# Kernel tuning notes

Measured on AMD Instinct MI355X. Metric: run time of the kernel, lower is better.

Reference implementation:

```python
import jax, jax.numpy as jnp
import numpy as np

B, HIST, PRED, N, E, FEAT = 16, 8, 12, 2000, 64000, 13
IN_DIM = FEAT + 1          # 14 (pm25 concat features)
HID, GNN_OUT, EH, EOUT = 64, 13, 32, 30


def setup_inputs() -> dict:
    key = jax.random.key(0)
    ks = jax.random.split(key, 14)
    pm25_hist = jax.random.normal(ks[0], (B, HIST, N, 1), jnp.float32)
    feature = jax.random.normal(ks[1], (B, HIST + PRED, N, FEAT), jnp.float32)
    edge_index = jax.random.randint(ks[2], (2, E), 0, N)
    dist = jax.random.uniform(ks[3], (E,), minval=10.0, maxval=500.0)
    direc = jax.random.uniform(ks[4], (E,), minval=0.0, maxval=360.0)
    edge_attr = jnp.stack([dist, direc], axis=-1).astype(jnp.float32)  # [E,2]
    wind_mean = jnp.array([3.0, 180.0], jnp.float32)
    wind_std = jnp.array([2.0, 100.0], jnp.float32)

    def w(k, shape):
        return (jax.random.normal(k, shape, jnp.float32) * 0.1)

    return {
        "pm25_hist": pm25_hist, "feature": feature,
        "edge_attr": edge_attr, "wind_mean": wind_mean, "wind_std": wind_std,
        "We1": w(ks[5], (2 * IN_DIM + 3, EH)), "be1": jnp.zeros((EH,), jnp.float32),
        "We2": w(ks[6], (EH, EOUT)), "be2": jnp.zeros((EOUT,), jnp.float32),
        "Wn": w(ks[7], (EOUT, GNN_OUT)), "bn": jnp.zeros((GNN_OUT,), jnp.float32),
        "W1": w(ks[8], (IN_DIM + GNN_OUT, HID)), "b1": jnp.zeros((HID,), jnp.float32),
        "W2": w(ks[9], (HID, HID)), "b2": jnp.zeros((HID,), jnp.float32),
        "W3": w(ks[10], (HID, HID)), "b3": jnp.zeros((HID,), jnp.float32),
        "Wo": w(ks[11], (HID, 1)), "bo": jnp.zeros((1,), jnp.float32),
        "edge_index": edge_index,
    }


def reference(pm25_hist, feature, edge_attr, wind_mean, wind_std,
              We1, be1, We2, be2, Wn, bn, W1, b1, W2, b2, W3, b3, Wo, bo,
              edge_index):
    src, tgt = edge_index[0], edge_index[1]
    # edge_attr normalization computed once at init in the torch module (unbiased std)
    attr_norm = (edge_attr - edge_attr.mean(0)) / edge_attr.std(0, ddof=1)  # [E,2]
    bsz, n_nodes = pm25_hist.shape[0], pm25_hist.shape[2]
    hist_len = pm25_hist.shape[1]
    n_edges = src.shape[0]

    def graph_gnn(x):  # x: [B,N,IN_DIM]
        ns = x[:, src]   # [B,E,D] gather
        nt = x[:, tgt]   # [B,E,D]
        wind = ns[..., -2:] * wind_std + wind_mean          # de-normalize wind feats
        speed, wdir = wind[..., 0], wind[..., 1]
        theta = jnp.abs(edge_attr[:, 1] - wdir)             # |city_direc - wind_direc|
        ew = jax.nn.relu(3.0 * speed * jnp.cos(theta) / edge_attr[:, 0])  # [B,E]
        an = jnp.broadcast_to(attr_norm, (bsz, n_edges, 2))
        e = jnp.concatenate([ns, nt, an, ew[..., None]], axis=-1)  # [B,E,2D+3]
        e = jax.nn.sigmoid(e @ We1 + be1)
        e = jax.nn.sigmoid(e @ We2 + be2)                    # [B,E,EOUT]
        z = jnp.zeros((bsz, n_nodes, e.shape[-1]), e.dtype)
        agg = z.at[:, tgt].add(e) - z.at[:, src].add(e)      # scatter_add - scatter_add
        return jax.nn.sigmoid(agg @ Wn + bn)                 # [B,N,GNN_OUT]

    feats = jnp.swapaxes(feature[:, hist_len:], 0, 1)        # [PRED,B,N,FEAT]

    def step(xn, ft):
        x = jnp.concatenate([xn, ft], axis=-1)               # [B,N,IN_DIM]
        g = graph_gnn(x)
        h = jnp.concatenate([g, x], axis=-1)                 # [B,N,IN_DIM+GNN_OUT]
        h = jax.nn.sigmoid(h @ W1 + b1)
        h = jax.nn.sigmoid(h @ W2 + b2)
        h = jax.nn.sigmoid(h @ W3 + b3)
        xn_new = h @ Wo + bo                                 # [B,N,1]
        return xn_new, xn_new

    _, preds = jax.lax.scan(step, pm25_hist[:, -1], feats)   # [PRED,B,N,1]
    return jnp.swapaxes(preds, 0, 1)                         # [B,PRED,N,1]
```

## Files before the change

### kernel.cpp

```cpp
#include <hip/hip_runtime.h>
#include <math.h>

#define BB 16
#define HIST 8
#define PRED 12
#define NN 2000
#define NE 64000
#define FEAT 13
#define IN_DIM 14
#define HID 64
#define GNN_OUT 13
#define EH 32
#define EOUT 30
#define EOUT_PAD 32
#define TSTEPS 20
#define EIN 31
#define SB 128

typedef unsigned int uint;
typedef unsigned short ushort;

__device__ __forceinline__ float sigmoidf_(float x) {
    return __builtin_amdgcn_rcpf(1.0f + __expf(-x));
}
// ... 89 lines not shown
    int* off = blockIdx.x ? offS : offT;
    int* cur = blockIdx.x ? curS : curT;
    __shared__ int part[256];
    int tid = threadIdx.x;
    int base = tid * 8;
    int v[8]; int s = 0;
#pragma unroll
    for (int k = 0; k < 8; ++k) {
        int idx = base + k;
        int d = (idx < NN) ? deg[idx] : 0;
        v[k] = d; s += d;
    }
    part[tid] = s;
    __syncthreads();
    for (int offn = 1; offn < 256; offn <<= 1) {
        int x = part[tid];
        int y = (tid >= offn) ? part[tid - offn] : 0;
        __syncthreads();
        part[tid] = x + y;
        __syncthreads();
    }
    int run = (tid > 0) ? part[tid - 1] : 0;
#pragma unroll
    for (int k = 0; k < 8; ++k) {
        int idx = base + k;
        if (idx < NN) { off[idx] = run; cur[idx] = run; }
        run += v[k];
    }
    if (tid == 255) off[NN] = run;
}

__global__ void fill_kernel(const int* __restrict__ edge_index,
                            int* __restrict__ curT, int* __restrict__ curS,
                            int* __restrict__ posT, int* __restrict__ listS_eid) {
    int e = blockIdx.x * 256 + threadIdx.x;
    if (e >= NE) return;
    int tg = edge_index[NE + e], s = edge_index[e];
    int p = atomicAdd(&curT[tg], 1);
    posT[e] = p;
    int q = atomicAdd(&curS[s], 1);
    listS_eid[q] = e;
}

__global__ void map_kernel(const int* __restrict__ listS_eid,
                           const int* __restrict__ posT,
                           int* __restrict__ listS_pos) {
    int k = blockIdx.x * 256 + threadIdx.x;
    if (k >= NE) return;
    listS_pos[k] = posT[listS_eid[k]];
}

__global__ void sort_kernel(const int* __restrict__ edge_index,
                            const float* __restrict__ edge_attr,
                            const int* __restrict__ posT,
                            int* __restrict__ srcT, int* __restrict__ tgT,
                            float* __restrict__ attrT) {
    int e = blockIdx.x * 256 + threadIdx.x;
    if (e >= NE) return;
    int p = posT[e];
    srcT[p] = edge_index[e];
    tgT[p] = edge_index[NE + e];
    attrT[2 * p]     = edge_attr[2 * e];
    attrT[2 * p + 1] = edge_attr[2 * e + 1];
}

__global__ void ce_kernel(const float* __restrict__ attrT,
                          const float* __restrict__ stats,
                          const float* __restrict__ We1,
                          const float* __restrict__ be1,
                          uint* __restrict__ Ce) {
    int p = blockIdx.x * 256 + threadIdx.x;
    if (p >= NE) return;
    float an0 = (attrT[2 * p]     - stats[0]) * stats[1];
    float an1 = (attrT[2 * p + 1] - stats[2]) * stats[3];
    float c[EH];
#pragma unroll
    for (int j = 0; j < EH; ++j)
        c[j] = fmaf(an0, We1[28 * EH + j], fmaf(an1, We1[29 * EH + j], be1[j]));
    uint* dst = Ce + (size_t)p * 16;
#pragma unroll
    for (int q = 0; q < 16; ++q) dst[q] = pack2(c[2 * q], c[2 * q + 1]);
}

__global__ __launch_bounds__(256) void proj_kernel(
    const float* __restrict__ xn, const float* __restrict__ feature,
    const float* __restrict__ We1,
    const float* __restrict__ wind_mean, const float* __restrict__ wind_std,
    uint* __restrict__ Ps, uint* __restrict__ Pt,
    float* __restrict__ spd3, float* __restrict__ wdirA, int t) {
    int i = blockIdx.x * 256 + threadIdx.x;
    if (i >= BB * NN) return;
    int b = i / NN, n = i % NN;
    int ht = HIST + t;
    float x[IN_DIM];
    x[0] = xn[i];
    const float* fr = feature + ((size_t)(b * TSTEPS + ht) * NN + n) * FEAT;
#pragma unroll
    for (int f = 0; f < FEAT; ++f) x[1 + f] = fr[f];

    float ps[EH], pt[EH];
#pragma unroll
    for (int j = 0; j < EH; ++j) { ps[j] = 0.f; pt[j] = 0.f; }
#pragma unroll
    for (int f = 0; f < IN_DIM; ++f) {
        float xv = x[f];
#pragma unroll
        for (int j = 0; j < EH; ++j) {
            ps[j] = fmaf(xv, We1[f * EH + j], ps[j]);
            pt[j] = fmaf(xv, We1[(IN_DIM + f) * EH + j], pt[j]);
        }
    }
    uint* pso = Ps + (size_t)i * 16;
    uint* pto = Pt + (size_t)i * 16;
#pragma unroll
    for (int q = 0; q < 16; ++q) {
        pso[q] = pack2(ps[2 * q], ps[2 * q + 1]);
        pto[q] = pack2(pt[2 * q], pt[2 * q + 1]);
    }
    spd3[i]  = 3.0f * fmaf(x[12], wind_std[0], wind_mean[0]);
    wdirA[i] = fmaf(x[13], wind_std[1], wind_mean[1]);
}

__global__ __launch_bounds__(256) void edge_kernel_v3(
    const uint* __restrict__ Ps, const uint* __restrict__ Pt,
    const uint* __restrict__ Ce,
    const float* __restrict__ We1,
    const float* __restrict__ We2, const float* __restrict__ be2,
    const int* __restrict__ srcT, const int* __restrict__ tgT,
    const float* __restrict__ attrT,
    const float* __restrict__ spd3, const float* __restrict__ wdirA,
    ushort* __restrict__ e_out) {
    int p = blockIdx.x * 256 + threadIdx.x;
    if (p >= NE) return;
    int b = blockIdx.y;
    int s  = srcT[p];
    int tg = tgT[p];
    float dist  = attrT[2 * p];
    float direc = attrT[2 * p + 1];
    float sp3 = spd3[b * NN + s];
    float wd  = wdirA[b * NN + s];
    float theta = fabsf(direc - wd);
    float ew = fmaxf(sp3 * cosf(theta) * __builtin_amdgcn_rcpf(dist), 0.0f);

    const uint4* ps4 = (const uint4*)(Ps + ((size_t)b * NN + s)  * 16);
    const uint4* pt4 = (const uint4*)(Pt + ((size_t)b * NN + tg) * 16);
    const uint4* ce4 = (const uint4*)(Ce + (size_t)p * 16);

    float h[EH];
#pragma unroll
    for (int q = 0; q < 4; ++q) {
        uint4 a = ps4[q], c = pt4[q], d = ce4[q];
        uint av[4] = {a.x, a.y, a.z, a.w};
        uint cv[4] = {c.x, c.y, c.z, c.w};
        uint dv[4] = {d.x, d.y, d.z, d.w};
#pragma unroll
        for (int m = 0; m < 4; ++m) {
            int j = q * 8 + m * 2;
            h[j]     = bflo(av[m]) + bflo(cv[m]) + bflo(dv[m]);
            h[j + 1] = bfhi(av[m]) + bfhi(cv[m]) + bfhi(dv[m]);
        }
    }
#pragma unroll
    for (int j = 0; j < EH; ++j)
        h[j] = sigmoidf_(fmaf(ew, We1[30 * EH + j], h[j]));

    float o[EOUT];
#pragma unroll
    for (int j = 0; j < EOUT; ++j) o[j] = be2[j];
#pragma unroll
    for (int i = 0; i < EH; ++i) {
        float x = h[i];
#pragma unroll
        for (int j = 0; j < EOUT; ++j) o[j] = fmaf(x, We2[i * EOUT + j], o[j]);
    }

    uint w[16];
#pragma unroll
    for (int j = 0; j < 15; ++j)
        w[j] = pack2(sigmoidf_(o[2 * j]), sigmoidf_(o[2 * j + 1]));
    w[15] = 0u;
    uint4* dst = (uint4*)(e_out + ((size_t)b * NE + (size_t)p) * EOUT_PAD);
    dst[0] = make_uint4(w[0],  w[1],  w[2],  w[3]);
    dst[1] = make_uint4(w[4],  w[5],  w[6],  w[7]);
    dst[2] = make_uint4(w[8],  w[9],  w[10], w[11]);
    dst[3] = make_uint4(w[12], w[13], w[14], w[15]);
}

__global__ __launch_bounds__(256) void node_kernel_v4(
    const ushort* __restrict__ e_out,
    const int* __restrict__ offT, const int* __restrict__ offS,
    const int* __restrict__ listS_pos,
    float* __restrict__ xn,
    const float* __restrict__ feature,
    const float* __restrict__ Wn, const float* __restrict__ bn,
    const float* __restrict__ W1, const float* __restrict__ b1,
    const float* __restrict__ W2, const float* __restrict__ b2,
    const float* __restrict__ W3, const float* __restrict__ b3,
    const float* __restrict__ Wo, const float* __restrict__ bo,
    const float* __restrict__ We1,
    const float* __restrict__ wind_mean, const float* __restrict__ wind_std,
    uint* __restrict__ Ps, uint* __restrict__ Pt,
    float* __restrict__ spd3, float* __restrict__ wdirA,
    float* __restrict__ out, int t) {
    int wid  = threadIdx.x >> 6;
    int lane = threadIdx.x & 63;
    int node = blockIdx.x * 4 + wid;
    int b = node / NN, n = node % NN;
    int r = lane >> 2;
    int c = lane & 3;
    int ht = HIST + t;

    const uint4* base4 = (const uint4*)(e_out + (size_t)b * NE * EOUT_PAD);

    float acc[8];
#pragma unroll
    for (int i = 0; i < 8; ++i) acc[i] = 0.0f;

    int k0 = offT[n], k1 = offT[n + 1];
    for (int k = k0 + r; k < k1; k += 16) {
        uint4 v = base4[(size_t)k * 4 + c];
        uint vv[4] = {v.x, v.y, v.z, v.w};
#pragma unroll
        for (int m = 0; m < 4; ++m) {
            acc[2 * m]     += bflo(vv[m]);
            acc[2 * m + 1] += bfhi(vv[m]);
        }
    }
    int q0 = offS[n], q1 = offS[n + 1];
    for (int k = q0 + r; k < q1; k += 16) {
        int row = listS_pos[k];
        uint4 v = base4[(size_t)row * 4 + c];
        uint vv[4] = {v.x, v.y, v.z, v.w};
#pragma unroll
        for (int m = 0; m < 4; ++m) {
            acc[2 * m]     -= bflo(vv[m]);
            acc[2 * m + 1] -= bfhi(vv[m]);
        }
    }
#pragma unroll
    for (int m = 4; m <= 32; m <<= 1) {
#pragma unroll
        for (int i = 0; i < 8; ++i) acc[i] += __shfl_xor(acc[i], m);
    }

    __shared__ float smAgg[4][EOUT_PAD];
    __shared__ float smHin[4][28];
    __shared__ float smH[4][HID];

    if (c == 0 && r < 4) {
#pragma unroll
        for (int i = 0; i < 8; ++i) smAgg[wid][r * 8 + i] = acc[i];
    }
    __syncthreads();

    const float* fr = feature + ((size_t)(b * TSTEPS + ht) * NN + n) * FEAT;
    if (lane < GNN_OUT) {
        float g = bn[lane];
#pragma unroll
        for (int k = 0; k < EOUT; ++k)
            g = fmaf(smAgg[wid][k], Wn[k * GNN_OUT + lane], g);
        smHin[wid][lane] = sigmoidf_(g);
    } else if (lane < GNN_OUT + IN_DIM) {
        smHin[wid][lane] = (lane == GNN_OUT) ? xn[node] : fr[lane - GNN_OUT - 1];
    }
    __syncthreads();

    float v = b1[lane];
#pragma unroll
    for (int k = 0; k < GNN_OUT + IN_DIM; ++k)
        v = fmaf(smHin[wid][k], W1[k * HID + lane], v);
    float hval = sigmoidf_(v);
    smH[wid][lane] = hval;
    __syncthreads();

    v = b2[lane];
#pragma unroll
    for (int k = 0; k < HID; ++k)
        v = fmaf(smH[wid][k], W2[k * HID + lane], v);
    hval = sigmoidf_(v);
    __syncthreads();
    smH[wid][lane] = hval;
    __syncthreads();

    v = b3[lane];
#pragma unroll
    for (int k = 0; k < HID; ++k)
        v = fmaf(smH[wid][k], W3[k * HID + lane], v);
    hval = sigmoidf_(v);

    float partial = hval * Wo[lane];
#pragma unroll
    for (int m = 32; m >= 1; m >>= 1)
        partial += __shfl_xor(partial, m);
    float rr = partial + bo[0];
    if (lane == 0) {
        out[((size_t)(b * PRED + t)) * NN + n] = rr;
        xn[node] = rr;
    }

    if (t < PRED - 1) {
        const float* fr2 = feature + ((size_t)(b * TSTEPS + ht + 1) * NN + n) * FEAT;
        float xv[IN_DIM];
        xv[0] = rr;
#pragma unroll
        for (int f = 0; f < FEAT; ++f) xv[1 + f] = fr2[f];
        int j = lane & 31;
        int rowbase = (lane < 32) ? 0 : IN_DIM;
        float p = 0.0f;
#pragma unroll
        for (int f = 0; f < IN_DIM; ++f)
            p = fmaf(xv[f], We1[(rowbase + f) * EH + j], p);
        float pp = __shfl_xor(p, 1);
        if (!(j & 1)) {
            uint packed = pack2(p, pp);
            uint* dst = (lane < 32 ? Ps : Pt) + (size_t)node * 16;
            dst[j >> 1] = packed;
        }
        if (lane == 0) {
            spd3[node]  = 3.0f * fmaf(xv[12], wind_std[0], wind_mean[0]);
            wdirA[node] = fmaf(xv[13], wind_std[1], wind_mean[1]);
        }
    }
}

__device__ __forceinline__ void compute_edge(
    int b, int e, int t,
    const float* __restrict__ xn, const float* __restrict__ feature,
    const float* __restrict__ edge_attr, const int* __restrict__ edge_index,
    const float* __restrict__ stats,
    const float* __restrict__ wind_mean, const float* __restrict__ wind_std,
    const float* __restrict__ We1, const float* __restrict__ be1,
    const float* __restrict__ We2, const float* __restrict__ be2,
    float* __restrict__ o) {
    int s  = edge_index[e];
    int tg = edge_index[NE + e];
    int ht = HIST + t;
    const float* fs  = feature + ((size_t)(b * TSTEPS + ht) * NN + s)  * FEAT;
    const float* ftg = feature + ((size_t)(b * TSTEPS + ht) * NN + tg) * FEAT;
    float ev[EIN];
    ev[0] = xn[b * NN + s];
#pragma unroll
    for (int f = 0; f < FEAT; ++f) ev[1 + f] = fs[f];
    ev[14] = xn[b * NN + tg];
#pragma unroll
    for (int f = 0; f < FEAT; ++f) ev[15 + f] = ftg[f];
    float dist  = edge_attr[2 * e];
    float direc = edge_attr[2 * e + 1];
    ev[28] = (dist  - stats[0]) * stats[1];
    ev[29] = (direc - stats[2]) * stats[3];
    float speed = ev[12] * wind_std[0] + wind_mean[0];
    float wdir  = ev[13] * wind_std[1] + wind_mean[1];
    float theta = fabsf(direc - wdir);
    float ew    = 3.0f * speed * cosf(theta) / dist;
    ev[30] = fmaxf(ew, 0.0f);
    float h[EH];
// ... 142 lines not shown
    const float* be1 = (const float*)d_in[6];
    const float* We2 = (const float*)d_in[7];
    const float* be2 = (const float*)d_in[8];
    const float* Wn  = (const float*)d_in[9];
    const float* bn  = (const float*)d_in[10];
    const float* W1  = (const float*)d_in[11];
    const float* b1  = (const float*)d_in[12];
    const float* W2  = (const float*)d_in[13];
    const float* b2  = (const float*)d_in[14];
    const float* W3  = (const float*)d_in[15];
    const float* b3  = (const float*)d_in[16];
    const float* Wo  = (const float*)d_in[17];
    const float* bo  = (const float*)d_in[18];
    const int* edge_index = (const int*)d_in[19];
    float* out = (float*)d_out;

    char* ws = (char*)d_ws;
    size_t off = 0;
    auto alloc = [&](size_t bytes) {
        void* p = ws + off;
        off = (off + bytes + 255) & ~(size_t)255;
        return p;
    };
    float*  xn    = (float*)alloc((size_t)BB * NN * sizeof(float));
    float*  stats = (float*)alloc(4 * sizeof(float));
    double* part  = (double*)alloc(4 * SB * sizeof(double));
    int* degT      = (int*)alloc(NN * sizeof(int));
    int* degS      = (int*)alloc(NN * sizeof(int));
    int* offT      = (int*)alloc((NN + 1) * sizeof(int));
    int* offS      = (int*)alloc((NN + 1) * sizeof(int));
    int* curT      = (int*)alloc(NN * sizeof(int));
    int* curS      = (int*)alloc(NN * sizeof(int));
    int* posT      = (int*)alloc(NE * sizeof(int));
    int* listS_eid = (int*)alloc(NE * sizeof(int));
    int* listS_pos = (int*)alloc(NE * sizeof(int));
    size_t v2_mark = off;
    int*   srcT  = (int*)alloc(NE * sizeof(int));
    int*   tgT   = (int*)alloc(NE * sizeof(int));
    float* attrT = (float*)alloc(2 * NE * sizeof(float));
    uint*  Ce    = (uint*)alloc((size_t)NE * 16 * sizeof(uint));
    uint*  Ps    = (uint*)alloc((size_t)BB * NN * 16 * sizeof(uint));
    uint*  Pt    = (uint*)alloc((size_t)BB * NN * 16 * sizeof(uint));
    float* spd3  = (float*)alloc((size_t)BB * NN * sizeof(float));
    float* wdirA = (float*)alloc((size_t)BB * NN * sizeof(float));
    size_t eout_bytes = (size_t)BB * NE * EOUT_PAD * sizeof(ushort);
    bool v3 = (ws_size >= off + eout_bytes);
    ushort* e_out = v3 ? (ushort*)(ws + off) : (ushort*)(ws + v2_mark);

    stats_partial<<<SB, 256, 0, stream>>>(edge_attr, part);
    stats_final<<<1, 128, 0, stream>>>(part, stats);
    init_xn<<<(BB * NN + 255) / 256, 256, 0, stream>>>(pm25, xn);
    hipMemsetAsync(degT, 0, NN * sizeof(int), stream);
    hipMemsetAsync(degS, 0, NN * sizeof(int), stream);
    count_kernel<<<(NE + 255) / 256, 256, 0, stream>>>(edge_index, degT, degS);
    scan2_kernel<<<2, 256, 0, stream>>>(degT, degS, offT, offS, curT, curS);
    fill_kernel<<<(NE + 255) / 256, 256, 0, stream>>>(edge_index, curT, curS, posT, listS_eid);
    map_kernel<<<(NE + 255) / 256, 256, 0, stream>>>(listS_eid, posT, listS_pos);

    if (v3) {
        sort_kernel<<<(NE + 255) / 256, 256, 0, stream>>>(edge_index, edge_attr, posT,
                                                          srcT, tgT, attrT);
        ce_kernel<<<(NE + 255) / 256, 256, 0, stream>>>(attrT, stats, We1, be1, Ce);
        proj_kernel<<<(BB * NN + 255) / 256, 256, 0, stream>>>(
            xn, feature, We1, wind_mean, wind_std, Ps, Pt, spd3, wdirA, 0);
        for (int t = 0; t < PRED; ++t) {
            dim3 eg((NE + 255) / 256, BB);
            edge_kernel_v3<<<eg, 256, 0, stream>>>(Ps, Pt, Ce, We1, We2, be2,
                                                   srcT, tgT, attrT, spd3, wdirA, e_out);
            node_kernel_v4<<<BB * NN / 4, 256, 0, stream>>>(
                e_out, offT, offS, listS_pos, xn, feature,
                Wn, bn, W1, b1, W2, b2, W3, b3, Wo, bo,
                We1, wind_mean, wind_std, Ps, Pt, spd3, wdirA, out, t);
        }
    } else {
        for (int t = 0; t < PRED; ++t) {
            dim3 eg((NE + 255) / 256, BB);
            edge_kernel_v2<<<eg, 256, 0, stream>>>(xn, feature, edge_attr, edge_index,
                                                   stats, wind_mean, wind_std,
                                                   We1, be1, We2, be2, posT, e_out, t);
            node_kernel_v2<<<(BB * NN + 255) / 256, 256, 0, stream>>>(
                e_out, offT, offS, listS_pos, xn, feature,
                Wn, bn, W1, b1, W2, b2, W3, b3, Wo, bo, out, t);
        }
    }
}
```

Measured before the change: 1.859 ms.

## Write edge outputs in both target- and source-sorted order for contiguous scatter reads

The edge kernel now writes each edge's packed output twice: once in target-sorted order and once at its source-sorted position, using a new per-edge position map built during CSR construction. The node kernel then reads the subtracted source-side contributions contiguously rather than through the listS_pos indirection. This removes the random gather in the node aggregation. In exchange it doubles edge-output write traffic and workspace use, and it only takes effect when the workspace is large enough.

```diff
diff --git a/kernel.cpp b/kernel.cpp
--- a/kernel.cpp
+++ b/kernel.cpp
@@ -145,13 +145,15 @@
 
 __global__ void fill_kernel(const int* __restrict__ edge_index,
                             int* __restrict__ curT, int* __restrict__ curS,
-                            int* __restrict__ posT, int* __restrict__ listS_eid) {
+                            int* __restrict__ posT, int* __restrict__ posS,
+                            int* __restrict__ listS_eid) {
     int e = blockIdx.x * 256 + threadIdx.x;
     if (e >= NE) return;
     int tg = edge_index[NE + e], s = edge_index[e];
     int p = atomicAdd(&curT[tg], 1);
     posT[e] = p;
     int q = atomicAdd(&curS[s], 1);
+    posS[e] = q;
     listS_eid[q] = e;
 }
 
@@ -165,9 +167,9 @@
 
 __global__ void sort_kernel(const int* __restrict__ edge_index,
                             const float* __restrict__ edge_attr,
-                            const int* __restrict__ posT,
+                            const int* __restrict__ posT, const int* __restrict__ posS,
                             int* __restrict__ srcT, int* __restrict__ tgT,
-                            float* __restrict__ attrT) {
+                            float* __restrict__ attrT, int* __restrict__ pSrc) {
     int e = blockIdx.x * 256 + threadIdx.x;
     if (e >= NE) return;
     int p = posT[e];
@@ -175,6 +177,7 @@
     tgT[p] = edge_index[NE + e];
     attrT[2 * p]     = edge_attr[2 * e];
     attrT[2 * p + 1] = edge_attr[2 * e + 1];
+    pSrc[p] = posS[e];
 }
 
 __global__ void ce_kernel(const float* __restrict__ attrT,
@@ -232,6 +235,89 @@
     }
     spd3[i]  = 3.0f * fmaf(x[12], wind_std[0], wind_mean[0]);
     wdirA[i] = fmaf(x[13], wind_std[1], wind_mean[1]);
+}
+
+__device__ __forceinline__ void edge_mlp(
+    int p, int b, int s, int tg,
+    const uint* __restrict__ Ps, const uint* __restrict__ Pt,
+    const uint* __restrict__ Ce,
+    const float* __restrict__ We1,
+    const float* __restrict__ We2, const float* __restrict__ be2,
+    const float* __restrict__ attrT,
+    const float* __restrict__ spd3, const float* __restrict__ wdirA,
+    uint* __restrict__ w ) {
+    float dist  = attrT[2 * p];
+    float direc = attrT[2 * p + 1];
+    float sp3 = spd3[b * NN + s];
+    float wd  = wdirA[b * NN + s];
+    float theta = fabsf(direc - wd);
+    float ew = fmaxf(sp3 * cosf(theta) * __builtin_amdgcn_rcpf(dist), 0.0f);
+
+    const uint4* ps4 = (const uint4*)(Ps + ((size_t)b * NN + s)  * 16);
+    const uint4* pt4 = (const uint4*)(Pt + ((size_t)b * NN + tg) * 16);
+    const uint4* ce4 = (const uint4*)(Ce + (size_t)p * 16);
+
+    float h[EH];
+#pragma unroll
+    for (int q = 0; q < 4; ++q) {
+        uint4 a = ps4[q], c = pt4[q], d = ce4[q];
+        uint av[4] = {a.x, a.y, a.z, a.w};
+        uint cv[4] = {c.x, c.y, c.z, c.w};
+        uint dv[4] = {d.x, d.y, d.z, d.w};
+#pragma unroll
+        for (int m = 0; m < 4; ++m) {
+            int j = q * 8 + m * 2;
+            h[j]     = bflo(av[m]) + bflo(cv[m]) + bflo(dv[m]);
+            h[j + 1] = bfhi(av[m]) + bfhi(cv[m]) + bfhi(dv[m]);
+        }
+    }
+#pragma unroll
+    for (int j = 0; j < EH; ++j)
+        h[j] = sigmoidf_(fmaf(ew, We1[30 * EH + j], h[j]));
+
+    float o[EOUT];
+#pragma unroll
+    for (int j = 0; j < EOUT; ++j) o[j] = be2[j];
+#pragma unroll
+    for (int i = 0; i < EH; ++i) {
+        float x = h[i];
+#pragma unroll
+        for (int j = 0; j < EOUT; ++j) o[j] = fmaf(x, We2[i * EOUT + j], o[j]);
+    }
+#pragma unroll
+    for (int j = 0; j < 15; ++j)
+        w[j] = pack2(sigmoidf_(o[2 * j]), sigmoidf_(o[2 * j + 1]));
+    w[15] = 0u;
+}
+
+__global__ __launch_bounds__(256) void edge_kernel_v5(
+    const uint* __restrict__ Ps, const uint* __restrict__ Pt,
+    const uint* __restrict__ Ce,
+    const float* __restrict__ We1,
+    const float* __restrict__ We2, const float* __restrict__ be2,
+    const int* __restrict__ srcT, const int* __restrict__ tgT,
+    const int* __restrict__ pSrc,
+    const float* __restrict__ attrT,
+    const float* __restrict__ spd3, const float* __restrict__ wdirA,
+    ushort* __restrict__ e_outT, ushort* __restrict__ e_outS) {
+    int p = blockIdx.x * 256 + threadIdx.x;
+    if (p >= NE) return;
+    int b = blockIdx.y;
+    int s  = srcT[p];
+    int tg = tgT[p];
+    uint w[16];
+    edge_mlp(p, b, s, tg, Ps, Pt, Ce, We1, We2, be2, attrT, spd3, wdirA, w);
+    uint4* dstT = (uint4*)(e_outT + ((size_t)b * NE + (size_t)p) * EOUT_PAD);
+    dstT[0] = make_uint4(w[0],  w[1],  w[2],  w[3]);
+    dstT[1] = make_uint4(w[4],  w[5],  w[6],  w[7]);
+    dstT[2] = make_uint4(w[8],  w[9],  w[10], w[11]);
+    dstT[3] = make_uint4(w[12], w[13], w[14], w[15]);
+    int q = pSrc[p];
+    uint4* dstS = (uint4*)(e_outS + ((size_t)b * NE + (size_t)q) * EOUT_PAD);
+    dstS[0] = make_uint4(w[0],  w[1],  w[2],  w[3]);
+    dstS[1] = make_uint4(w[4],  w[5],  w[6],  w[7]);
+    dstS[2] = make_uint4(w[8],  w[9],  w[10], w[11]);
+    dstS[3] = make_uint4(w[12], w[13], w[14], w[15]);
 }
 
 __global__ __launch_bounds__(256) void edge_kernel_v3(
@@ -248,55 +334,169 @@
     int b = blockIdx.y;
     int s  = srcT[p];
     int tg = tgT[p];
-    float dist  = attrT[2 * p];
-    float direc = attrT[2 * p + 1];
-    float sp3 = spd3[b * NN + s];
-    float wd  = wdirA[b * NN + s];
-    float theta = fabsf(direc - wd);
-    float ew = fmaxf(sp3 * cosf(theta) * __builtin_amdgcn_rcpf(dist), 0.0f);
-
-    const uint4* ps4 = (const uint4*)(Ps + ((size_t)b * NN + s)  * 16);
-    const uint4* pt4 = (const uint4*)(Pt + ((size_t)b * NN + tg) * 16);
-    const uint4* ce4 = (const uint4*)(Ce + (size_t)p * 16);
-
-    float h[EH];
-#pragma unroll
-    for (int q = 0; q < 4; ++q) {
-        uint4 a = ps4[q], c = pt4[q], d = ce4[q];
-        uint av[4] = {a.x, a.y, a.z, a.w};
-        uint cv[4] = {c.x, c.y, c.z, c.w};
-        uint dv[4] = {d.x, d.y, d.z, d.w};
-#pragma unroll
-        for (int m = 0; m < 4; ++m) {
-            int j = q * 8 + m * 2;
-            h[j]     = bflo(av[m]) + bflo(cv[m]) + bflo(dv[m]);
-            h[j + 1] = bfhi(av[m]) + bfhi(cv[m]) + bfhi(dv[m]);
-        }
-    }
-#pragma unroll
-    for (int j = 0; j < EH; ++j)
-        h[j] = sigmoidf_(fmaf(ew, We1[30 * EH + j], h[j]));
-
-    float o[EOUT];
-#pragma unroll
-    for (int j = 0; j < EOUT; ++j) o[j] = be2[j];
-#pragma unroll
-    for (int i = 0; i < EH; ++i) {
-        float x = h[i];
-#pragma unroll
-        for (int j = 0; j < EOUT; ++j) o[j] = fmaf(x, We2[i * EOUT + j], o[j]);
-    }
-
     uint w[16];
-#pragma unroll
-    for (int j = 0; j < 15; ++j)
-        w[j] = pack2(sigmoidf_(o[2 * j]), sigmoidf_(o[2 * j + 1]));
-    w[15] = 0u;
+    edge_mlp(p, b, s, tg, Ps, Pt, Ce, We1, We2, be2, attrT, spd3, wdirA, w);
     uint4* dst = (uint4*)(e_out + ((size_t)b * NE + (size_t)p) * EOUT_PAD);
     dst[0] = make_uint4(w[0],  w[1],  w[2],  w[3]);
     dst[1] = make_uint4(w[4],  w[5],  w[6],  w[7]);
     dst[2] = make_uint4(w[8],  w[9],  w[10], w[11]);
     dst[3] = make_uint4(w[12], w[13], w[14], w[15]);
+}
+
+__device__ __forceinline__ void node_tail(
+    int node, int b, int n, int t, int wid, int lane,
+    float accv[8], int r, int c,
+    float* __restrict__ xn, const float* __restrict__ feature,
+    const float* __restrict__ Wn, const float* __restrict__ bn,
+    const float* __restrict__ W1, const float* __restrict__ b1,
+    const float* __restrict__ W2, const float* __restrict__ b2,
+    const float* __restrict__ W3, const float* __restrict__ b3,
+    const float* __restrict__ Wo, const float* __restrict__ bo,
+    const float* __restrict__ We1,
+    const float* __restrict__ wind_mean, const float* __restrict__ wind_std,
+    uint* __restrict__ Ps, uint* __restrict__ Pt,
+    float* __restrict__ spd3, float* __restrict__ wdirA,
+    float* __restrict__ out,
+    float (*smAgg)[EOUT_PAD], float (*smHin)[28], float (*smH)[HID]) {
+    int ht = HIST + t;
+#pragma unroll
+    for (int m = 4; m <= 32; m <<= 1) {
+#pragma unroll
+        for (int i = 0; i < 8; ++i) accv[i] += __shfl_xor(accv[i], m);
+    }
+    if (c == 0 && r < 4) {
+#pragma unroll
+        for (int i = 0; i < 8; ++i) smAgg[wid][r * 8 + i] = accv[i];
+    }
+    __syncthreads();
+
+    const float* fr = feature + ((size_t)(b * TSTEPS + ht) * NN + n) * FEAT;
+    if (lane < GNN_OUT) {
+        float g = bn[lane];
+#pragma unroll
+        for (int k = 0; k < EOUT; ++k)
+            g = fmaf(smAgg[wid][k], Wn[k * GNN_OUT + lane], g);
+        smHin[wid][lane] = sigmoidf_(g);
+    } else if (lane < GNN_OUT + IN_DIM) {
+        smHin[wid][lane] = (lane == GNN_OUT) ? xn[node] : fr[lane - GNN_OUT - 1];
+    }
+    __syncthreads();
+
+    float v = b1[lane];
+#pragma unroll
+    for (int k = 0; k < GNN_OUT + IN_DIM; ++k)
+        v = fmaf(smHin[wid][k], W1[k * HID + lane], v);
+    float hval = sigmoidf_(v);
+    smH[wid][lane] = hval;
+    __syncthreads();
+
+    v = b2[lane];
+#pragma unroll
+    for (int k = 0; k < HID; ++k)
+        v = fmaf(smH[wid][k], W2[k * HID + lane], v);
+    hval = sigmoidf_(v);
+    __syncthreads();
+    smH[wid][lane] = hval;
+    __syncthreads();
+
+    v = b3[lane];
+#pragma unroll
+    for (int k = 0; k < HID; ++k)
+        v = fmaf(smH[wid][k], W3[k * HID + lane], v);
+    hval = sigmoidf_(v);
+
+    float partial = hval * Wo[lane];
+#pragma unroll
+    for (int m = 32; m >= 1; m >>= 1)
+        partial += __shfl_xor(partial, m);
+    float rr = partial + bo[0];
+    if (lane == 0) {
+        out[((size_t)(b * PRED + t)) * NN + n] = rr;
+        xn[node] = rr;
+    }
+
+    if (t < PRED - 1) {
+        const float* fr2 = feature + ((size_t)(b * TSTEPS + ht + 1) * NN + n) * FEAT;
+        float xv[IN_DIM];
+        xv[0] = rr;
+#pragma unroll
+        for (int f = 0; f < FEAT; ++f) xv[1 + f] = fr2[f];
+        int j = lane & 31;
+        int rowbase = (lane < 32) ? 0 : IN_DIM;
+        float p = 0.0f;
+#pragma unroll
+        for (int f = 0; f < IN_DIM; ++f)
+            p = fmaf(xv[f], We1[(rowbase + f) * EH + j], p);
+        float pp = __shfl_xor(p, 1);
+        if (!(j & 1)) {
+            uint packed = pack2(p, pp);
+            uint* dst = (lane < 32 ? Ps : Pt) + (size_t)node * 16;
+            dst[j >> 1] = packed;
+        }
+        if (lane == 0) {
+            spd3[node]  = 3.0f * fmaf(xv[12], wind_std[0], wind_mean[0]);
+            wdirA[node] = fmaf(xv[13], wind_std[1], wind_mean[1]);
+        }
+    }
+}
+
+__global__ __launch_bounds__(256) void node_kernel_v5(
+    const ushort* __restrict__ e_outT, const ushort* __restrict__ e_outS,
+    const int* __restrict__ offT, const int* __restrict__ offS,
+    float* __restrict__ xn,
+    const float* __restrict__ feature,
+    const float* __restrict__ Wn, const float* __restrict__ bn,
+    const float* __restrict__ W1, const float* __restrict__ b1,
+    const float* __restrict__ W2, const float* __restrict__ b2,
+    const float* __restrict__ W3, const float* __restrict__ b3,
+    const float* __restrict__ Wo, const float* __restrict__ bo,
+    const float* __restrict__ We1,
+    const float* __restrict__ wind_mean, const float* __restrict__ wind_std,
+    uint* __restrict__ Ps, uint* __restrict__ Pt,
+    float* __restrict__ spd3, float* __restrict__ wdirA,
+    float* __restrict__ out, int t) {
+    int wid  = threadIdx.x >> 6;
+    int lane = threadIdx.x & 63;
+    int node = blockIdx.x * 4 + wid;
+    int b = node / NN, n = node % NN;
+    int r = lane >> 2;
+    int c = lane & 3;
+
+    const uint4* baseT4 = (const uint4*)(e_outT + (size_t)b * NE * EOUT_PAD);
+    const uint4* baseS4 = (const uint4*)(e_outS + (size_t)b * NE * EOUT_PAD);
+
+    float acc[8];
+#pragma unroll
+    for (int i = 0; i < 8; ++i) acc[i] = 0.0f;
+
+    int k0 = offT[n], k1 = offT[n + 1];
+    for (int k = k0 + r; k < k1; k += 16) {
+        uint4 v = baseT4[(size_t)k * 4 + c];
+        uint vv[4] = {v.x, v.y, v.z, v.w};
+#pragma unroll
+        for (int m = 0; m < 4; ++m) {
+            acc[2 * m]     += bflo(vv[m]);
+            acc[2 * m + 1] += bfhi(vv[m]);
+        }
+    }
+    int q0 = offS[n], q1 = offS[n + 1];
+    for (int k = q0 + r; k < q1; k += 16) {
+        uint4 v = baseS4[(size_t)k * 4 + c];
+        uint vv[4] = {v.x, v.y, v.z, v.w};
+#pragma unroll
+        for (int m = 0; m < 4; ++m) {
+            acc[2 * m]     -= bflo(vv[m]);
+            acc[2 * m + 1] -= bfhi(vv[m]);
+        }
+    }
+
+    __shared__ float smAgg[4][EOUT_PAD];
+    __shared__ float smHin[4][28];
+    __shared__ float smH[4][HID];
+    node_tail(node, b, n, t, wid, lane, acc, r, c, xn, feature,
+              Wn, bn, W1, b1, W2, b2, W3, b3, Wo, bo,
+              We1, wind_mean, wind_std, Ps, Pt, spd3, wdirA, out,
+              smAgg, smHin, smH);
 }
 
 __global__ __launch_bounds__(256) void node_kernel_v4(
@@ -321,7 +521,6 @@
     int b = node / NN, n = node % NN;
     int r = lane >> 2;
     int c = lane & 3;
-    int ht = HIST + t;
 
     const uint4* base4 = (const uint4*)(e_out + (size_t)b * NE * EOUT_PAD);
 
@@ -350,90 +549,14 @@
             acc[2 * m + 1] -= bfhi(vv[m]);
         }
     }
-#pragma unroll
-    for (int m = 4; m <= 32; m <<= 1) {
-#pragma unroll
-        for (int i = 0; i < 8; ++i) acc[i] += __shfl_xor(acc[i], m);
-    }
 
     __shared__ float smAgg[4][EOUT_PAD];
     __shared__ float smHin[4][28];
     __shared__ float smH[4][HID];
-
-    if (c == 0 && r < 4) {
-#pragma unroll
-        for (int i = 0; i < 8; ++i) smAgg[wid][r * 8 + i] = acc[i];
-    }
-    __syncthreads();
-
-    const float* fr = feature + ((size_t)(b * TSTEPS + ht) * NN + n) * FEAT;
-    if (lane < GNN_OUT) {
-        float g = bn[lane];
-#pragma unroll
-        for (int k = 0; k < EOUT; ++k)
-            g = fmaf(smAgg[wid][k], Wn[k * GNN_OUT + lane], g);
-        smHin[wid][lane] = sigmoidf_(g);
-    } else if (lane < GNN_OUT + IN_DIM) {
-        smHin[wid][lane] = (lane == GNN_OUT) ? xn[node] : fr[lane - GNN_OUT - 1];
-    }
-    __syncthreads();
-
-    float v = b1[lane];
-#pragma unroll
-    for (int k = 0; k < GNN_OUT + IN_DIM; ++k)
-        v = fmaf(smHin[wid][k], W1[k * HID + lane], v);
-    float hval = sigmoidf_(v);
-    smH[wid][lane] = hval;
-    __syncthreads();
-
-    v = b2[lane];
-#pragma unroll
-    for (int k = 0; k < HID; ++k)
-        v = fmaf(smH[wid][k], W2[k * HID + lane], v);
-    hval = sigmoidf_(v);
-    __syncthreads();
-    smH[wid][lane] = hval;
-    __syncthreads();
-
-    v = b3[lane];
-#pragma unroll
-    for (int k = 0; k < HID; ++k)
-        v = fmaf(smH[wid][k], W3[k * HID + lane], v);
-    hval = sigmoidf_(v);
-
-    float partial = hval * Wo[lane];
-#pragma unroll
-    for (int m = 32; m >= 1; m >>= 1)
-        partial += __shfl_xor(partial, m);
-    float rr = partial + bo[0];
-    if (lane == 0) {
-        out[((size_t)(b * PRED + t)) * NN + n] = rr;
-        xn[node] = rr;
-    }
-
-    if (t < PRED - 1) {
-        const float* fr2 = feature + ((size_t)(b * TSTEPS + ht + 1) * NN + n) * FEAT;
-        float xv[IN_DIM];
-        xv[0] = rr;
-#pragma unroll
-        for (int f = 0; f < FEAT; ++f) xv[1 + f] = fr2[f];
-        int j = lane & 31;
-        int rowbase = (lane < 32) ? 0 : IN_DIM;
-        float p = 0.0f;
-#pragma unroll
-        for (int f = 0; f < IN_DIM; ++f)
-            p = fmaf(xv[f], We1[(rowbase + f) * EH + j], p);
-        float pp = __shfl_xor(p, 1);
-        if (!(j & 1)) {
-            uint packed = pack2(p, pp);
-            uint* dst = (lane < 32 ? Ps : Pt) + (size_t)node * 16;
-            dst[j >> 1] = packed;
-        }
-        if (lane == 0) {
-            spd3[node]  = 3.0f * fmaf(xv[12], wind_std[0], wind_mean[0]);
-            wdirA[node] = fmaf(xv[13], wind_std[1], wind_mean[1]);
-        }
-    }
+    node_tail(node, b, n, t, wid, lane, acc, r, c, xn, feature,
+              Wn, bn, W1, b1, W2, b2, W3, b3, Wo, bo,
+              We1, wind_mean, wind_std, Ps, Pt, spd3, wdirA, out,
+              smAgg, smHin, smH);
 }
 
 __device__ __forceinline__ void compute_edge(
@@ -642,20 +765,27 @@
     int* curT      = (int*)alloc(NN * sizeof(int));
     int* curS      = (int*)alloc(NN * sizeof(int));
     int* posT      = (int*)alloc(NE * sizeof(int));
+    int* posS      = (int*)alloc(NE * sizeof(int));
     int* listS_eid = (int*)alloc(NE * sizeof(int));
     int* listS_pos = (int*)alloc(NE * sizeof(int));
     size_t v2_mark = off;
     int*   srcT  = (int*)alloc(NE * sizeof(int));
     int*   tgT   = (int*)alloc(NE * sizeof(int));
+    int*   pSrc  = (int*)alloc(NE * sizeof(int));
     float* attrT = (float*)alloc(2 * NE * sizeof(float));
     uint*  Ce    = (uint*)alloc((size_t)NE * 16 * sizeof(uint));
     uint*  Ps    = (uint*)alloc((size_t)BB * NN * 16 * sizeof(uint));
     uint*  Pt    = (uint*)alloc((size_t)BB * NN * 16 * sizeof(uint));
     float* spd3  = (float*)alloc((size_t)BB * NN * sizeof(float));
     float* wdirA = (float*)alloc((size_t)BB * NN * sizeof(float));
+    size_t base_off = off;
     size_t eout_bytes = (size_t)BB * NE * EOUT_PAD * sizeof(ushort);
-    bool v3 = (ws_size >= off + eout_bytes);
-    ushort* e_out = v3 ? (ushort*)(ws + off) : (ushort*)(ws + v2_mark);
+
+    bool v5 = (ws_size >= base_off + 2 * eout_bytes);
+    bool v3 = !v5 && (ws_size >= base_off + eout_bytes);
+    ushort* e_outT = (ushort*)(ws + base_off);
+    ushort* e_outS = (ushort*)(ws + base_off + eout_bytes);
+    if (!v5 && !v3) e_outT = (ushort*)(ws + v2_mark);
 
     stats_partial<<<SB, 256, 0, stream>>>(edge_attr, part);
     stats_final<<<1, 128, 0, stream>>>(part, stats);
@@ -664,32 +794,45 @@
     hipMemsetAsync(degS, 0, NN * sizeof(int), stream);
     count_kernel<<<(NE + 255) / 256, 256, 0, stream>>>(edge_index, degT, degS);
     scan2_kernel<<<2, 256, 0, stream>>>(degT, degS, offT, offS, curT, curS);
-    fill_kernel<<<(NE + 255) / 256, 256, 0, stream>>>(edge_index, curT, curS, posT, listS_eid);
+    fill_kernel<<<(NE + 255) / 256, 256, 0, stream>>>(edge_index, curT, curS,
+                                                      posT, posS, listS_eid);
     map_kernel<<<(NE + 255) / 256, 256, 0, stream>>>(listS_eid, posT, listS_pos);
 
-    if (v3) {
-        sort_kernel<<<(NE + 255) / 256, 256, 0, stream>>>(edge_index, edge_attr, posT,
-                                                          srcT, tgT, attrT);
+    if (v5 || v3) {
+        sort_kernel<<<(NE + 255) / 256, 256, 0, stream>>>(edge_index, edge_attr,
+                                                          posT, posS,
+                                                          srcT, tgT, attrT, pSrc);
         ce_kernel<<<(NE + 255) / 256, 256, 0, stream>>>(attrT, stats, We1, be1, Ce);
         proj_kernel<<<(BB * NN + 255) / 256, 256, 0, stream>>>(
             xn, feature, We1, wind_mean, wind_std, Ps, Pt, spd3, wdirA, 0);
+        dim3 eg((NE + 255) / 256, BB);
         for (int t = 0; t < PRED; ++t) {
-            dim3 eg((NE + 255) / 256, BB);
-            edge_kernel_v3<<<eg, 256, 0, stream>>>(Ps, Pt, Ce, We1, We2, be2,
-                                                   srcT, tgT, attrT, spd3, wdirA, e_out);
-            node_kernel_v4<<<BB * NN / 4, 256, 0, stream>>>(
-                e_out, offT, offS, listS_pos, xn, feature,
-                Wn, bn, W1, b1, W2, b2, W3, b3, Wo, bo,
-                We1, wind_mean, wind_std, Ps, Pt, spd3, wdirA, out, t);
+            if (v5) {
+                edge_kernel_v5<<<eg, 256, 0, stream>>>(Ps, Pt, Ce, We1, We2, be2,
+                                                       srcT, tgT, pSrc, attrT,
+                                                       spd3, wdirA, e_outT, e_outS);
+                node_kernel_v5<<<BB * NN / 4, 256, 0, stream>>>(
+                    e_outT, e_outS, offT, offS, xn, feature,
+                    Wn, bn, W1, b1, W2, b2, W3, b3, Wo, bo,
+                    We1, wind_mean, wind_std, Ps, Pt, spd3, wdirA, out, t);
+            } else {
+                edge_kernel_v3<<<eg, 256, 0, stream>>>(Ps, Pt, Ce, We1, We2, be2,
+                                                       srcT, tgT, attrT,
+                                                       spd3, wdirA, e_outT);
+                node_kernel_v4<<<BB * NN / 4, 256, 0, stream>>>(
+                    e_outT, offT, offS, listS_pos, xn, feature,
+                    Wn, bn, W1, b1, W2, b2, W3, b3, Wo, bo,
+                    We1, wind_mean, wind_std, Ps, Pt, spd3, wdirA, out, t);
+            }
         }
     } else {
         for (int t = 0; t < PRED; ++t) {
             dim3 eg((NE + 255) / 256, BB);
             edge_kernel_v2<<<eg, 256, 0, stream>>>(xn, feature, edge_attr, edge_index,
                                                    stats, wind_mean, wind_std,
-                                                   We1, be1, We2, be2, posT, e_out, t);
+                                                   We1, be1, We2, be2, posT, e_outT, t);
             node_kernel_v2<<<(BB * NN + 255) / 256, 256, 0, stream>>>(
-                e_out, offT, offS, listS_pos, xn, feature,
+                e_outT, offT, offS, listS_pos, xn, feature,
                 Wn, bn, W1, b1, W2, b2, W3, b3, Wo, bo, out, t);
         }
     }
```

Result: slower. 1.954 ms (+5.1%).

## Interleave batch dimension innermost for node projections and edge outputs

Applied to the files above, without the earlier changes.

Moves the batch index to the innermost position of Ps/Pt, the wind arrays and e_out, so the 16 batch lanes for one edge or node touch adjacent memory. The edge kernel maps 16 threads per edge across the batches, and the node kernel gives each block one node for all 16 batches. Each gathered CSR row then becomes one contiguous segment instead of 16 scattered ones, which should improve coalescing and cache reuse of the srcT/tgT/Ce loads. The node MLP now runs in four serialized passes with extra block barriers, which lowers parallelism within the node phase.

```diff
diff --git a/kernel.cpp b/kernel.cpp
--- a/kernel.cpp
+++ b/kernel.cpp
@@ -195,19 +195,18 @@
     for (int q = 0; q < 16; ++q) dst[q] = pack2(c[2 * q], c[2 * q + 1]);
 }
 
-__global__ __launch_bounds__(256) void proj_kernel(
+__global__ __launch_bounds__(256) void proj0_kernel(
     const float* __restrict__ xn, const float* __restrict__ feature,
     const float* __restrict__ We1,
     const float* __restrict__ wind_mean, const float* __restrict__ wind_std,
     uint* __restrict__ Ps, uint* __restrict__ Pt,
-    float* __restrict__ spd3, float* __restrict__ wdirA, int t) {
+    float* __restrict__ spd3, float* __restrict__ wdirA) {
     int i = blockIdx.x * 256 + threadIdx.x;
     if (i >= BB * NN) return;
     int b = i / NN, n = i % NN;
-    int ht = HIST + t;
     float x[IN_DIM];
     x[0] = xn[i];
-    const float* fr = feature + ((size_t)(b * TSTEPS + ht) * NN + n) * FEAT;
+    const float* fr = feature + ((size_t)(b * TSTEPS + HIST) * NN + n) * FEAT;
 #pragma unroll
     for (int f = 0; f < FEAT; ++f) x[1 + f] = fr[f];
 
@@ -223,18 +222,18 @@
             pt[j] = fmaf(xv, We1[(IN_DIM + f) * EH + j], pt[j]);
         }
     }
-    uint* pso = Ps + (size_t)i * 16;
-    uint* pto = Pt + (size_t)i * 16;
+    uint* pso = Ps + ((size_t)n * BB + b) * 16;
+    uint* pto = Pt + ((size_t)n * BB + b) * 16;
 #pragma unroll
     for (int q = 0; q < 16; ++q) {
         pso[q] = pack2(ps[2 * q], ps[2 * q + 1]);
         pto[q] = pack2(pt[2 * q], pt[2 * q + 1]);
     }
-    spd3[i]  = 3.0f * fmaf(x[12], wind_std[0], wind_mean[0]);
-    wdirA[i] = fmaf(x[13], wind_std[1], wind_mean[1]);
-}
-
-__global__ __launch_bounds__(256) void edge_kernel_v3(
+    spd3[n * BB + b]  = 3.0f * fmaf(x[12], wind_std[0], wind_mean[0]);
+    wdirA[n * BB + b] = fmaf(x[13], wind_std[1], wind_mean[1]);
+}
+
+__global__ __launch_bounds__(256) void edge_kernel_v6(
     const uint* __restrict__ Ps, const uint* __restrict__ Pt,
     const uint* __restrict__ Ce,
     const float* __restrict__ We1,
@@ -243,20 +242,20 @@
     const float* __restrict__ attrT,
     const float* __restrict__ spd3, const float* __restrict__ wdirA,
     ushort* __restrict__ e_out) {
-    int p = blockIdx.x * 256 + threadIdx.x;
-    if (p >= NE) return;
-    int b = blockIdx.y;
+    int tid = threadIdx.x;
+    int b = tid & 15;
+    int p = blockIdx.x * 16 + (tid >> 4);
     int s  = srcT[p];
     int tg = tgT[p];
     float dist  = attrT[2 * p];
     float direc = attrT[2 * p + 1];
-    float sp3 = spd3[b * NN + s];
-    float wd  = wdirA[b * NN + s];
+    float sp3 = spd3[s * BB + b];
+    float wd  = wdirA[s * BB + b];
     float theta = fabsf(direc - wd);
     float ew = fmaxf(sp3 * cosf(theta) * __builtin_amdgcn_rcpf(dist), 0.0f);
 
-    const uint4* ps4 = (const uint4*)(Ps + ((size_t)b * NN + s)  * 16);
-    const uint4* pt4 = (const uint4*)(Pt + ((size_t)b * NN + tg) * 16);
+    const uint4* ps4 = (const uint4*)(Ps + ((size_t)s  * BB + b) * 16);
+    const uint4* pt4 = (const uint4*)(Pt + ((size_t)tg * BB + b) * 16);
     const uint4* ce4 = (const uint4*)(Ce + (size_t)p * 16);
 
     float h[EH];
@@ -292,14 +291,14 @@
     for (int j = 0; j < 15; ++j)
         w[j] = pack2(sigmoidf_(o[2 * j]), sigmoidf_(o[2 * j + 1]));
     w[15] = 0u;
-    uint4* dst = (uint4*)(e_out + ((size_t)b * NE + (size_t)p) * EOUT_PAD);
+    uint4* dst = (uint4*)(e_out + ((size_t)p * BB + b) * EOUT_PAD);
     dst[0] = make_uint4(w[0],  w[1],  w[2],  w[3]);
     dst[1] = make_uint4(w[4],  w[5],  w[6],  w[7]);
     dst[2] = make_uint4(w[8],  w[9],  w[10], w[11]);
     dst[3] = make_uint4(w[12], w[13], w[14], w[15]);
 }
 
-__global__ __launch_bounds__(256) void node_kernel_v4(
+__global__ __launch_bounds__(256) void node_kernel_v6(
     const ushort* __restrict__ e_out,
     const int* __restrict__ offT, const int* __restrict__ offS,
     const int* __restrict__ listS_pos,
@@ -315,124 +314,164 @@
     uint* __restrict__ Ps, uint* __restrict__ Pt,
     float* __restrict__ spd3, float* __restrict__ wdirA,
     float* __restrict__ out, int t) {
-    int wid  = threadIdx.x >> 6;
-    int lane = threadIdx.x & 63;
-    int node = blockIdx.x * 4 + wid;
-    int b = node / NN, n = node % NN;
-    int r = lane >> 2;
-    int c = lane & 3;
+    int n = blockIdx.x;
+    int tid = threadIdx.x;
+    int w = tid >> 6;
+    int lane = tid & 63;
+    int b = lane & 15;
+    int c = lane >> 4;
     int ht = HIST + t;
 
-    const uint4* base4 = (const uint4*)(e_out + (size_t)b * NE * EOUT_PAD);
-
-    float acc[8];
-#pragma unroll
-    for (int i = 0; i < 8; ++i) acc[i] = 0.0f;
+    const uint4* base4 = (const uint4*)e_out;
+
+    float accA[8], accB[8];
+#pragma unroll
+    for (int i = 0; i < 8; ++i) { accA[i] = 0.f; accB[i] = 0.f; }
 
     int k0 = offT[n], k1 = offT[n + 1];
-    for (int k = k0 + r; k < k1; k += 16) {
-        uint4 v = base4[(size_t)k * 4 + c];
-        uint vv[4] = {v.x, v.y, v.z, v.w};
+    int k = k0 + w;
+    for (; k + 4 < k1; k += 8) {
+        uint4 v0 = base4[((size_t)k       * BB + b) * 4 + c];
+        uint4 v1 = base4[((size_t)(k + 4) * BB + b) * 4 + c];
+        uint a0[4] = {v0.x, v0.y, v0.z, v0.w};
+        uint a1[4] = {v1.x, v1.y, v1.z, v1.w};
 #pragma unroll
         for (int m = 0; m < 4; ++m) {
-            acc[2 * m]     += bflo(vv[m]);
-            acc[2 * m + 1] += bfhi(vv[m]);
+            accA[2 * m]     += bflo(a0[m]);
+            accA[2 * m + 1] += bfhi(a0[m]);
+            accB[2 * m]     += bflo(a1[m]);
+            accB[2 * m + 1] += bfhi(a1[m]);
+        }
+    }
+    for (; k < k1; k += 4) {
+        uint4 v0 = base4[((size_t)k * BB + b) * 4 + c];
+        uint a0[4] = {v0.x, v0.y, v0.z, v0.w};
+#pragma unroll
+        for (int m = 0; m < 4; ++m) {
+            accA[2 * m]     += bflo(a0[m]);
+            accA[2 * m + 1] += bfhi(a0[m]);
         }
     }
     int q0 = offS[n], q1 = offS[n + 1];
-    for (int k = q0 + r; k < q1; k += 16) {
-        int row = listS_pos[k];
-        uint4 v = base4[(size_t)row * 4 + c];
-        uint vv[4] = {v.x, v.y, v.z, v.w};
+    k = q0 + w;
+    for (; k + 4 < q1; k += 8) {
+        int r0 = listS_pos[k];
+        int r1 = listS_pos[k + 4];
+        uint4 v0 = base4[((size_t)r0 * BB + b) * 4 + c];
+        uint4 v1 = base4[((size_t)r1 * BB + b) * 4 + c];
+        uint a0[4] = {v0.x, v0.y, v0.z, v0.w};
+        uint a1[4] = {v1.x, v1.y, v1.z, v1.w};
 #pragma unroll
         for (int m = 0; m < 4; ++m) {
-            acc[2 * m]     -= bflo(vv[m]);
-            acc[2 * m + 1] -= bfhi(vv[m]);
-        }
-    }
-#pragma unroll
-    for (int m = 4; m <= 32; m <<= 1) {
-#pragma unroll
-        for (int i = 0; i < 8; ++i) acc[i] += __shfl_xor(acc[i], m);
-    }
-
-    __shared__ float smAgg[4][EOUT_PAD];
-    __shared__ float smHin[4][28];
-    __shared__ float smH[4][HID];
-
-    if (c == 0 && r < 4) {
-#pragma unroll
-        for (int i = 0; i < 8; ++i) smAgg[wid][r * 8 + i] = acc[i];
-    }
+            accA[2 * m]     -= bflo(a0[m]);
+            accA[2 * m + 1] -= bfhi(a0[m]);
+            accB[2 * m]     -= bflo(a1[m]);
+            accB[2 * m + 1] -= bfhi(a1[m]);
+        }
+    }
+    for (; k < q1; k += 4) {
+        int r0 = listS_pos[k];
+        uint4 v0 = base4[((size_t)r0 * BB + b) * 4 + c];
+        uint a0[4] = {v0.x, v0.y, v0.z, v0.w};
+#pragma unroll
+        for (int m = 0; m < 4; ++m) {
+            accA[2 * m]     -= bflo(a0[m]);
+            accA[2 * m + 1] -= bfhi(a0[m]);
+        }
+    }
+
+    __shared__ float smAcc[4][16][36];
+    __shared__ float smAgg[16][36];
+    __shared__ float smHin[16][28];
+    __shared__ float smH[16][HID];
+
+#pragma unroll
+    for (int i = 0; i < 8; ++i) smAcc[w][b][c * 8 + i] = accA[i] + accB[i];
     __syncthreads();
 
-    const float* fr = feature + ((size_t)(b * TSTEPS + ht) * NN + n) * FEAT;
-    if (lane < GNN_OUT) {
-        float g = bn[lane];
-#pragma unroll
-        for (int k = 0; k < EOUT; ++k)
-            g = fmaf(smAgg[wid][k], Wn[k * GNN_OUT + lane], g);
-        smHin[wid][lane] = sigmoidf_(g);
-    } else if (lane < GNN_OUT + IN_DIM) {
-        smHin[wid][lane] = (lane == GNN_OUT) ? xn[node] : fr[lane - GNN_OUT - 1];
+    {
+        int col = tid & 31, bb = tid >> 5;
+        smAgg[bb][col] = smAcc[0][bb][col] + smAcc[1][bb][col]
+                       + smAcc[2][bb][col] + smAcc[3][bb][col];
+        int b2 = bb + 8;
+        smAgg[b2][col] = smAcc[0][b2][col] + smAcc[1][b2][col]
+                       + smAcc[2][b2][col] + smAcc[3][b2][col];
     }
     __syncthreads();
 
-    float v = b1[lane];
-#pragma unroll
-    for (int k = 0; k < GNN_OUT + IN_DIM; ++k)
-        v = fmaf(smHin[wid][k], W1[k * HID + lane], v);
-    float hval = sigmoidf_(v);
-    smH[wid][lane] = hval;
-    __syncthreads();
-
-    v = b2[lane];
-#pragma unroll
-    for (int k = 0; k < HID; ++k)
-        v = fmaf(smH[wid][k], W2[k * HID + lane], v);
-    hval = sigmoidf_(v);
-    __syncthreads();
-    smH[wid][lane] = hval;
-    __syncthreads();
-
-    v = b3[lane];
-#pragma unroll
-    for (int k = 0; k < HID; ++k)
-        v = fmaf(smH[wid][k], W3[k * HID + lane], v);
-    hval = sigmoidf_(v);
-
-    float partial = hval * Wo[lane];
-#pragma unroll
-    for (int m = 32; m >= 1; m >>= 1)
-        partial += __shfl_xor(partial, m);
-    float rr = partial + bo[0];
-    if (lane == 0) {
-        out[((size_t)(b * PRED + t)) * NN + n] = rr;
-        xn[node] = rr;
-    }
-
-    if (t < PRED - 1) {
-        const float* fr2 = feature + ((size_t)(b * TSTEPS + ht + 1) * NN + n) * FEAT;
-        float xv[IN_DIM];
-        xv[0] = rr;
-#pragma unroll
-        for (int f = 0; f < FEAT; ++f) xv[1 + f] = fr2[f];
-        int j = lane & 31;
-        int rowbase = (lane < 32) ? 0 : IN_DIM;
-        float p = 0.0f;
-#pragma unroll
-        for (int f = 0; f < IN_DIM; ++f)
-            p = fmaf(xv[f], We1[(rowbase + f) * EH + j], p);
-        float pp = __shfl_xor(p, 1);
-        if (!(j & 1)) {
-            uint packed = pack2(p, pp);
-            uint* dst = (lane < 32 ? Ps : Pt) + (size_t)node * 16;
-            dst[j >> 1] = packed;
-        }
+#pragma unroll
+    for (int pass = 0; pass < 4; ++pass) {
+        int bb = pass * 4 + w;
+        const float* fr = feature + ((size_t)(bb * TSTEPS + ht) * NN + n) * FEAT;
+        if (lane < GNN_OUT) {
+            float g = bn[lane];
+#pragma unroll
+            for (int kk = 0; kk < EOUT; ++kk)
+                g = fmaf(smAgg[bb][kk], Wn[kk * GNN_OUT + lane], g);
+            smHin[bb][lane] = sigmoidf_(g);
+        } else if (lane < GNN_OUT + IN_DIM) {
+            smHin[bb][lane] = (lane == GNN_OUT) ? xn[bb * NN + n]
+                                                : fr[lane - GNN_OUT - 1];
+        }
+        __syncthreads();
+
+        float v = b1[lane];
+#pragma unroll
+        for (int kk = 0; kk < GNN_OUT + IN_DIM; ++kk)
+            v = fmaf(smHin[bb][kk], W1[kk * HID + lane], v);
+        float hval = sigmoidf_(v);
+        smH[bb][lane] = hval;
+        __syncthreads();
+
+        v = b2[lane];
+#pragma unroll
+        for (int kk = 0; kk < HID; ++kk)
+            v = fmaf(smH[bb][kk], W2[kk * HID + lane], v);
+        hval = sigmoidf_(v);
+        __syncthreads();
+        smH[bb][lane] = hval;
+        __syncthreads();
+
+        v = b3[lane];
+#pragma unroll
+        for (int kk = 0; kk < HID; ++kk)
+            v = fmaf(smH[bb][kk], W3[kk * HID + lane], v);
+        hval = sigmoidf_(v);
+
+        float partial = hval * Wo[lane];
+#pragma unroll
+        for (int m = 32; m >= 1; m >>= 1)
+            partial += __shfl_xor(partial, m);
+        float rr = partial + bo[0];
         if (lane == 0) {
-            spd3[node]  = 3.0f * fmaf(xv[12], wind_std[0], wind_mean[0]);
-            wdirA[node] = fmaf(xv[13], wind_std[1], wind_mean[1]);
-        }
+            out[((size_t)(bb * PRED + t)) * NN + n] = rr;
+            xn[bb * NN + n] = rr;
+        }
+
+        if (t < PRED - 1) {
+            const float* fr2 = feature + ((size_t)(bb * TSTEPS + ht + 1) * NN + n) * FEAT;
+            float xv[IN_DIM];
+            xv[0] = rr;
+#pragma unroll
+            for (int f = 0; f < FEAT; ++f) xv[1 + f] = fr2[f];
+            int j = lane & 31;
+            int rowbase = (lane < 32) ? 0 : IN_DIM;
+            float p = 0.0f;
+#pragma unroll
+            for (int f = 0; f < IN_DIM; ++f)
+                p = fmaf(xv[f], We1[(rowbase + f) * EH + j], p);
+            float pp = __shfl_xor(p, 1);
+            if (!(j & 1)) {
+                uint packed = pack2(p, pp);
+                uint* dst = (lane < 32 ? Ps : Pt) + ((size_t)n * BB + bb) * 16;
+                dst[j >> 1] = packed;
+            }
+            if (lane == 0) {
+                spd3[n * BB + bb]  = 3.0f * fmaf(xv[12], wind_std[0], wind_mean[0]);
+                wdirA[n * BB + bb] = fmaf(xv[13], wind_std[1], wind_mean[1]);
+            }
+        }
+        __syncthreads();
     }
 }
 
@@ -649,13 +688,15 @@
     int*   tgT   = (int*)alloc(NE * sizeof(int));
     float* attrT = (float*)alloc(2 * NE * sizeof(float));
     uint*  Ce    = (uint*)alloc((size_t)NE * 16 * sizeof(uint));
-    uint*  Ps    = (uint*)alloc((size_t)BB * NN * 16 * sizeof(uint));
-    uint*  Pt    = (uint*)alloc((size_t)BB * NN * 16 * sizeof(uint));
-    float* spd3  = (float*)alloc((size_t)BB * NN * sizeof(float));
-    float* wdirA = (float*)alloc((size_t)BB * NN * sizeof(float));
-    size_t eout_bytes = (size_t)BB * NE * EOUT_PAD * sizeof(ushort);
-    bool v3 = (ws_size >= off + eout_bytes);
-    ushort* e_out = v3 ? (ushort*)(ws + off) : (ushort*)(ws + v2_mark);
+    uint*  Ps    = (uint*)alloc((size_t)NN * BB * 16 * sizeof(uint));
+    uint*  Pt    = (uint*)alloc((size_t)NN * BB * 16 * sizeof(uint));
+    float* spd3  = (float*)alloc((size_t)NN * BB * sizeof(float));
+    float* wdirA = (float*)alloc((size_t)NN * BB * sizeof(float));
+    size_t base_off = off;
+    size_t eout_bytes = (size_t)NE * BB * EOUT_PAD * sizeof(ushort);
+
+    bool v6 = (ws_size >= base_off + eout_bytes);
+    ushort* e_out = v6 ? (ushort*)(ws + base_off) : (ushort*)(ws + v2_mark);
 
     stats_partial<<<SB, 256, 0, stream>>>(edge_attr, part);
     stats_final<<<1, 128, 0, stream>>>(part, stats);
@@ -664,20 +705,21 @@
     hipMemsetAsync(degS, 0, NN * sizeof(int), stream);
     count_kernel<<<(NE + 255) / 256, 256, 0, stream>>>(edge_index, degT, degS);
     scan2_kernel<<<2, 256, 0, stream>>>(degT, degS, offT, offS, curT, curS);
-    fill_kernel<<<(NE + 255) / 256, 256, 0, stream>>>(edge_index, curT, curS, posT, listS_eid);
+    fill_kernel<<<(NE + 255) / 256, 256, 0, stream>>>(edge_index, curT, curS,
+                                                      posT, listS_eid);
     map_kernel<<<(NE + 255) / 256, 256, 0, stream>>>(listS_eid, posT, listS_pos);
 
-    if (v3) {
+    if (v6) {
         sort_kernel<<<(NE + 255) / 256, 256, 0, stream>>>(edge_index, edge_attr, posT,
                                                           srcT, tgT, attrT);
         ce_kernel<<<(NE + 255) / 256, 256, 0, stream>>>(attrT, stats, We1, be1, Ce);
-        proj_kernel<<<(BB * NN + 255) / 256, 256, 0, stream>>>(
-            xn, feature, We1, wind_mean, wind_std, Ps, Pt, spd3, wdirA, 0);
+        proj0_kernel<<<(BB * NN + 255) / 256, 256, 0, stream>>>(
+            xn, feature, We1, wind_mean, wind_std, Ps, Pt, spd3, wdirA);
         for (int t = 0; t < PRED; ++t) {
-            dim3 eg((NE + 255) / 256, BB);
-            edge_kernel_v3<<<eg, 256, 0, stream>>>(Ps, Pt, Ce, We1, We2, be2,
-                                                   srcT, tgT, attrT, spd3, wdirA, e_out);
-            node_kernel_v4<<<BB * NN / 4, 256, 0, stream>>>(
+            edge_kernel_v6<<<NE / 16, 256, 0, stream>>>(Ps, Pt, Ce, We1, We2, be2,
+                                                        srcT, tgT, attrT,
+                                                        spd3, wdirA, e_out);
+            node_kernel_v6<<<NN, 256, 0, stream>>>(
                 e_out, offT, offS, listS_pos, xn, feature,
                 Wn, bn, W1, b1, W2, b2, W3, b3, Wo, bo,
                 We1, wind_mean, wind_std, Ps, Pt, spd3, wdirA, out, t);
```

Result: slower. 5.183 ms (+178.8%).
